# Performance work log

Measured on AMD Instinct MI355X. Metric: run time of the kernel, lower is better.

The kernel has to match this reference:

```python
import jax, jax.numpy as jnp
import numpy as np

N = 100000          # nodes
E = 1200000         # edges
IN_DIM = 128
HID = 64
NUM_CLASSES = 5
NUM_GRAPHS = 128


def setup_inputs() -> dict:
    key = jax.random.key(0)
    ks = jax.random.split(key, 12)
    x = jax.random.normal(ks[0], (N, IN_DIM), dtype=jnp.float32)
    edge_index = jax.random.randint(ks[1], (2, E), 0, N, dtype=jnp.int64)
    batch = jnp.sort(jax.random.randint(ks[2], (N,), 0, NUM_GRAPHS, dtype=jnp.int64))
    def glorot(k, shape):
        lim = np.sqrt(6.0 / (shape[0] + shape[1]))
        return jax.random.uniform(k, shape, jnp.float32, -lim, lim)
    W1 = glorot(ks[3], (IN_DIM, HID)); b1 = jnp.zeros((HID,), jnp.float32)
    W2 = glorot(ks[4], (HID, HID));    b2 = jnp.zeros((HID,), jnp.float32)
    W3 = glorot(ks[5], (HID, HID));    b3 = jnp.zeros((HID,), jnp.float32)
    Wc = glorot(ks[6], (HID, NUM_CLASSES)); bc = jnp.zeros((NUM_CLASSES,), jnp.float32)
    return {"x": x, "edge_index": edge_index, "batch": batch,
            "W1": W1, "b1": b1, "W2": W2, "b2": b2, "W3": W3, "b3": b3,
            "Wc": Wc, "bc": bc}


def _gcn_norm(edge_index, n_nodes):
    # PyG GCNConv: add self-loops, symmetric normalization D^-1/2 (A+I) D^-1/2
    loop = jnp.arange(n_nodes, dtype=edge_index.dtype)
    src = jnp.concatenate([edge_index[0], loop])  # [E+N]
    dst = jnp.concatenate([edge_index[1], loop])
    deg = jax.ops.segment_sum(jnp.ones_like(dst, dtype=jnp.float32), dst,
                              num_segments=n_nodes)
    dinv = jnp.where(deg > 0, jax.lax.rsqrt(deg), 0.0)
    norm = dinv[src] * dinv[dst]                   # [E+N]
    return src, dst, norm


def _gcn_conv(x, src, dst, norm, W, b, n_nodes):
    h = x @ W                                      # [N, out]
    msg = h[src] * norm[:, None]                   # gather + scale
    agg = jax.ops.segment_sum(msg, dst, num_segments=n_nodes)  # scatter-add
    return agg + b


def reference(x, edge_index, batch, W1, b1, W2, b2, W3, b3, Wc, bc):
    src, dst, norm = _gcn_norm(edge_index, N)
    h = jax.nn.relu(_gcn_conv(x, src, dst, norm, W1, b1, N))
    h = jax.nn.relu(_gcn_conv(h, src, dst, norm, W2, b2, N))
    h = jax.nn.relu(_gcn_conv(h, src, dst, norm, W3, b3, N))
    # global_mean_pool over batch ids
    sums = jax.ops.segment_sum(h, batch, num_segments=NUM_GRAPHS)
    counts = jax.ops.segment_sum(jnp.ones((N,), jnp.float32), batch,
                                 num_segments=NUM_GRAPHS)
    pooled = sums / jnp.maximum(counts, 1.0)[:, None]  # [G, HID]
    return pooled @ Wc + bc                             # [G, num_classes]
```

## Files before the change

kernel.cpp:

```cpp
#include <hip/hip_runtime.h>
#include <hip/hip_bf16.h>

#define NN 100000
#define NE 1200000
#define IND 128
#define HID 64
#define NC 5
#define NG 128
#define NB 391
#define GB 1172
#define G1 3125

static __device__ __forceinline__ float bf2f(unsigned short u) {
    union { unsigned int i; float f; } x;
    x.i = (unsigned int)u << 16;
    return x.f;
}
static __device__ __forceinline__ unsigned short f2bf(float f) {
    union { float f; unsigned int i; } x;
    x.f = f;
    unsigned int r = (x.i + 0x7fffu + ((x.i >> 16) & 1u)) >> 16;
    return (unsigned short)r;
}

__global__ __launch_bounds__(256) void k_hist(const int* __restrict__ dst, int* __restrict__ cnt,
                                              int* __restrict__ rank) {
    int e = blockIdx.x * 256 + threadIdx.x;
    if (e < NE) rank[e] = atomicAdd(&cnt[dst[e]], 1);
}

__global__ __launch_bounds__(256) void k_scan1(const int* __restrict__ cnt, int* __restrict__ exc,
                                               int* __restrict__ bsum, float* __restrict__ dinv) {
    __shared__ int lds[256];
    int tid = threadIdx.x;
    int i = blockIdx.x * 256 + tid;
    int v = (i < NN) ? cnt[i] : 0;
    lds[tid] = v;
    __syncthreads();
    for (int off = 1; off < 256; off <<= 1) {
        int t = (tid >= off) ? lds[tid - off] : 0;
        __syncthreads();
        lds[tid] += t;
        __syncthreads();
    }
    if (i < NN) {
        exc[i] = lds[tid] - v;
        dinv[i] = rsqrtf((float)v + 1.0f);
    }
    if (tid == 255) bsum[blockIdx.x] = lds[255];
}

__global__ __launch_bounds__(512) void k_scan2(int* __restrict__ bsum) {
    __shared__ int lds[512];
    int tid = threadIdx.x;
    int v = (tid < NB) ? bsum[tid] : 0;
    lds[tid] = v;
    __syncthreads();
    for (int off = 1; off < 512; off <<= 1) {
        int t = (tid >= off) ? lds[tid - off] : 0;
        __syncthreads();
        lds[tid] += t;
        __syncthreads();
    }
    if (tid < NB) bsum[tid] = lds[tid] - v;
}

__global__ __launch_bounds__(256) void k_scan3(const int* __restrict__ exc, const int* __restrict__ bsum,
                                               int* __restrict__ row_ptr) {
    int i = blockIdx.x * 256 + threadIdx.x;
    if (i < NN) row_ptr[i] = exc[i] + bsum[blockIdx.x];
    if (i == 0) row_ptr[NN] = NE;
}

__global__ __launch_bounds__(256) void k_fused1(
    const float* __restrict__ X, const float* __restrict__ W,
    const float* __restrict__ dinv, unsigned short* __restrict__ out_bf,
    const int* __restrict__ src, const int* __restrict__ dst,
    const int* __restrict__ row_ptr, const int* __restrict__ rank,
    int* __restrict__ src_sorted,
    const int* __restrict__ batch, int* __restrict__ start)
{
    __shared__ float lds[IND * HID + 32 * IND];
    int tid = threadIdx.x;

    if (blockIdx.x < GB) {
        int t = blockIdx.x * 256 + tid;
        const int T = GB * 256;
#pragma unroll
        for (int u = 0; u < 4; ++u) {
            int e = t + u * T;
            if (e < NE) src_sorted[row_ptr[dst[e]] + rank[e]] = src[e];
        }
        return;
    }
    if (blockIdx.x >= GB + G1) {
        int i = (blockIdx.x - GB - G1) * 256 + tid;
        if (i >= NN) return;
        int b = batch[i];
        if (i == 0) {
            for (int g = 0; g <= b; ++g) start[g] = 0;
        } else {
            int p = batch[i - 1];
            for (int g = p + 1; g <= b; ++g) start[g] = i;
        }
        if (i == NN - 1) {
            for (int g = b + 1; g <= NG; ++g) start[g] = NN;
        }
        return;
    }

    float* Wl = lds;
    float* xl = lds + IND * HID;
    int n0 = (blockIdx.x - GB) * 32;
    int c = tid & 31;
    int s = tid >> 5;

    {
        const float4* Wg = (const float4*)W;
        float4* Wl4 = (float4*)Wl;
#pragma unroll
        for (int i = 0; i < IND * 16 / 256; ++i) Wl4[i * 256 + tid] = Wg[i * 256 + tid];
    }
    {
        const float4* Xg = (const float4*)X;
        float4* xl4 = (float4*)xl;
        const float4 z = {0.f, 0.f, 0.f, 0.f};
#pragma unroll
        for (int i = 0; i < 32 * IND / 4 / 256; ++i) {
            int idx = i * 256 + tid;
            int node = n0 + idx / (IND / 4);
            xl4[idx] = (node < NN) ? Xg[(size_t)n0 * (IND / 4) + idx] : z;
        }
    }
    __syncthreads();

    float acc[4][2];
#pragma unroll
    for (int r = 0; r < 4; ++r) { acc[r][0] = 0.f; acc[r][1] = 0.f; }

#pragma unroll 4
    for (int k0 = 0; k0 < IND; k0 += 4) {
        float4 xv[4];
#pragma unroll
        for (int r = 0; r < 4; ++r) xv[r] = *(const float4*)&xl[(s * 4 + r) * IND + k0];
#pragma unroll
        for (int kk = 0; kk < 4; ++kk) {
            float w0 = Wl[(k0 + kk) * HID + c];
            float w1 = Wl[(k0 + kk) * HID + c + 32];
#pragma unroll
            for (int r = 0; r < 4; ++r) {
                float xe = (kk == 0) ? xv[r].x : (kk == 1) ? xv[r].y : (kk == 2) ? xv[r].z : xv[r].w;
                acc[r][0] = fmaf(xe, w0, acc[r][0]);
                acc[r][1] = fmaf(xe, w1, acc[r][1]);
            }
        }
    }

#pragma unroll
    for (int r = 0; r < 4; ++r) {
        int n = n0 + s * 4 + r;
        if (n < NN) {
            float dn = dinv[n];
            out_bf[n * HID + c]      = f2bf(acc[r][0] * dn);
            out_bf[n * HID + c + 32] = f2bf(acc[r][1] * dn);
        }
    }
}

__global__ __launch_bounds__(256) void k_aggregate(const unsigned short* __restrict__ hW,
                                                   const int* __restrict__ srcs,
                                                   const int* __restrict__ row_ptr,
                                                   const float* __restrict__ dinv,
                                                   const float* __restrict__ b,
                                                   unsigned short* __restrict__ outb) {
    int tid = threadIdx.x;
    int j = tid & 63;
    int n = blockIdx.x * 4 + (tid >> 6);
    if (n >= NN) return;
    float acc = bf2f(hW[n * HID + j]);
    int beg = row_ptr[n], end = row_ptr[n + 1];
    int e = beg;
    for (; e + 7 < end; e += 8) {
        int s0 = srcs[e],     s1 = srcs[e + 1], s2 = srcs[e + 2], s3 = srcs[e + 3];
        int s4 = srcs[e + 4], s5 = srcs[e + 5], s6 = srcs[e + 6], s7 = srcs[e + 7];
        float h0 = bf2f(hW[s0 * HID + j]);
        float h1 = bf2f(hW[s1 * HID + j]);
        float h2 = bf2f(hW[s2 * HID + j]);
        float h3 = bf2f(hW[s3 * HID + j]);
        float h4 = bf2f(hW[s4 * HID + j]);
        float h5 = bf2f(hW[s5 * HID + j]);
        float h6 = bf2f(hW[s6 * HID + j]);
        float h7 = bf2f(hW[s7 * HID + j]);
        acc += ((h0 + h1) + (h2 + h3)) + ((h4 + h5) + (h6 + h7));
    }
    if (e + 3 < end) {
        int s0 = srcs[e], s1 = srcs[e + 1], s2 = srcs[e + 2], s3 = srcs[e + 3];
        float h0 = bf2f(hW[s0 * HID + j]);
        float h1 = bf2f(hW[s1 * HID + j]);
        float h2 = bf2f(hW[s2 * HID + j]);
        float h3 = bf2f(hW[s3 * HID + j]);
        acc += (h0 + h1) + (h2 + h3);
        e += 4;
    }
    for (; e < end; ++e) acc += bf2f(hW[srcs[e] * HID + j]);
    outb[n * HID + j] = f2bf(fmaxf(fmaf(dinv[n], acc, b[j]), 0.0f));
}

__global__ __launch_bounds__(256) void k_gemm_bf(const unsigned short* __restrict__ X,
                                                 const float* __restrict__ W,
                                                 const float* __restrict__ dinv,
                                                 unsigned short* __restrict__ outb) {
    __shared__ float Wl[HID * HID];
    __shared__ float xl[64 * HID];
    int tid = threadIdx.x;
    int n0 = blockIdx.x * 64;

    {
        const float4* Wg = (const float4*)W;
        float4* Wl4 = (float4*)Wl;
#pragma unroll
        for (int i = 0; i < HID * HID / 4 / 256; ++i) Wl4[i * 256 + tid] = Wg[i * 256 + tid];
    }
    {
        const uint4* Xg = (const uint4*)X;
#pragma unroll
        for (int i = 0; i < 2; ++i) {
            int idx = i * 256 + tid;
            int ln = idx >> 3;
            int k0 = (idx & 7) * 8;
            int node = n0 + ln;
            float f[8];
            if (node < NN) {
                uint4 u = Xg[(size_t)n0 * 8 + idx];
                f[0] = bf2f((unsigned short)(u.x & 0xffff));
                f[1] = bf2f((unsigned short)(u.x >> 16));
                f[2] = bf2f((unsigned short)(u.y & 0xffff));
                f[3] = bf2f((unsigned short)(u.y >> 16));
                f[4] = bf2f((unsigned short)(u.z & 0xffff));
                f[5] = bf2f((unsigned short)(u.z >> 16));
                f[6] = bf2f((unsigned short)(u.w & 0xffff));
                f[7] = bf2f((unsigned short)(u.w >> 16));
            } else {
#pragma unroll
                for (int q = 0; q < 8; ++q) f[q] = 0.f;
            }
#pragma unroll
            for (int q = 0; q < 8; ++q) xl[ln * HID + k0 + q] = f[q];
        }
    }
    __syncthreads();

    int c = tid & 31;
    int s = tid >> 5;
    float acc[8][2];
#pragma unroll
    for (int r = 0; r < 8; ++r) { acc[r][0] = 0.f; acc[r][1] = 0.f; }

#pragma unroll 4
    for (int k0 = 0; k0 < HID; k0 += 4) {
        float4 xv[8];
#pragma unroll
        for (int r = 0; r < 8; ++r) xv[r] = *(const float4*)&xl[(s * 8 + r) * HID + k0];
#pragma unroll
        for (int kk = 0; kk < 4; ++kk) {
            float w0 = Wl[(k0 + kk) * HID + c];
            float w1 = Wl[(k0 + kk) * HID + c + 32];
#pragma unroll
            for (int r = 0; r < 8; ++r) {
                float xe = (kk == 0) ? xv[r].x : (kk == 1) ? xv[r].y : (kk == 2) ? xv[r].z : xv[r].w;
                acc[r][0] = fmaf(xe, w0, acc[r][0]);
                acc[r][1] = fmaf(xe, w1, acc[r][1]);
            }
        }
    }

#pragma unroll
    for (int r = 0; r < 8; ++r) {
        int n = n0 + s * 8 + r;
        if (n < NN) {
            float dn = dinv[n];
            outb[n * HID + c]      = f2bf(acc[r][0] * dn);
            outb[n * HID + c + 32] = f2bf(acc[r][1] * dn);
        }
    }
}

__global__ __launch_bounds__(256) void k_pool_head(const unsigned short* __restrict__ h,
                                                   const int* __restrict__ start,
                                                   const float* __restrict__ Wc, const float* __restrict__ bc,
                                                   float* __restrict__ out) {
    __shared__ float part[4][HID];
    int g = blockIdx.x;
    int tid = threadIdx.x;
    int j = tid & 63, w = tid >> 6;
    int beg = start[g], end = start[g + 1];
    float acc = 0.0f;
    for (int n = beg + w; n < end; n += 4) acc += bf2f(h[n * HID + j]);
    part[w][j] = acc;
    __syncthreads();
    if (w == 0) {
        float s = part[0][j] + part[1][j] + part[2][j] + part[3][j];
        float cnt = (float)(end - beg);
        float p = s / fmaxf(cnt, 1.0f);
#pragma unroll
        for (int c = 0; c < NC; ++c) {
            float v = p * Wc[j * NC + c];
            for (int off = 32; off > 0; off >>= 1) v += __shfl_down(v, off);
            if (j == 0) out[g * NC + c] = v + bc[c];
        }
    }
}

extern "C" void kernel_launch(void* const* d_in, const int* in_sizes, int n_in,
                              void* d_out, int out_size, void* d_ws, size_t ws_size,
                              hipStream_t stream) {
    const float* x  = (const float*)d_in[0];
    const int* ei   = (const int*)d_in[1];
    const int* bat  = (const int*)d_in[2];
    const float* W1 = (const float*)d_in[3];
    const float* b1 = (const float*)d_in[4];
    const float* W2 = (const float*)d_in[5];
    const float* b2 = (const float*)d_in[6];
    const float* W3 = (const float*)d_in[7];
    const float* b3 = (const float*)d_in[8];
    const float* Wc = (const float*)d_in[9];
    const float* bc = (const float*)d_in[10];
    float* out = (float*)d_out;

    const int* src = ei;
    const int* dst = ei + NE;

    char* wsb = (char*)d_ws;
    float* dinv         = (float*)wsb;
    int*   row_ptr      = (int*)(wsb + 400000);
    int*   srcs         = (int*)(wsb + 800016);
    unsigned short* hWA = (unsigned short*)(wsb + 5600016);
    unsigned short* hWB = (unsigned short*)(wsb + 18400016);
    int*   cnt          = (int*)(wsb + 31200016);
    int*   exc          = (int*)(wsb + 31600016);
    int*   bsum         = (int*)(wsb + 32000016);
    int*   rank         = (int*)(wsb + 32002064);
    int*   start        = (int*)(wsb + 36802064);

    const int gE = (NE + 255) / 256;

    hipMemsetAsync(cnt, 0, NN * sizeof(int), stream);
    k_hist<<<gE, 256, 0, stream>>>(dst, cnt, rank);
    k_scan1<<<NB, 256, 0, stream>>>(cnt, exc, bsum, dinv);
    k_scan2<<<1, 512, 0, stream>>>(bsum);
    k_scan3<<<NB, 256, 0, stream>>>(exc, bsum, row_ptr);

    k_fused1<<<GB + G1 + NB, 256, 0, stream>>>(x, W1, dinv, hWA, src, dst, row_ptr, rank, srcs, bat, start);

    k_aggregate<<<NN / 4, 256, 0, stream>>>(hWA, srcs, row_ptr, dinv, b1, hWB);
    k_gemm_bf<<<(NN + 63) / 64, 256, 0, stream>>>(hWB, W2, dinv, hWA);
    k_aggregate<<<NN / 4, 256, 0, stream>>>(hWA, srcs, row_ptr, dinv, b2, hWB);
    k_gemm_bf<<<(NN + 63) / 64, 256, 0, stream>>>(hWB, W3, dinv, hWA);
    k_aggregate<<<NN / 4, 256, 0, stream>>>(hWA, srcs, row_ptr, dinv, b3, hWB);

    k_pool_head<<<NG, 256, 0, stream>>>(hWB, start, Wc, bc, out);
}
```

Measured before the change: 369.5 us.

## Merge scan passes and split aggregate gathers into packed bf16 pairs across half-wavefronts

Two changes. The second and third scan kernels become one: each block reduces the preceding block sums itself, which removes a single-block launch and a dependency. The aggregate kernel now has each half-wavefront load packed 32-bit bf16 pairs for alternating edges and combines the halves with a cross-lane shuffle. This halves the load instructions per edge and keeps two independent gathers in flight per thread. The cost is the shuffle and the idle half-wave during the epilogue.

Result: faster. 356.0 us (-3.6%).

```diff
diff --git a/kernel.cpp b/kernel.cpp
--- a/kernel.cpp
+++ b/kernel.cpp
@@ -50,25 +50,23 @@
     if (tid == 255) bsum[blockIdx.x] = lds[255];
 }
 
-__global__ __launch_bounds__(512) void k_scan2(int* __restrict__ bsum) {
-    __shared__ int lds[512];
-    int tid = threadIdx.x;
-    int v = (tid < NB) ? bsum[tid] : 0;
+__global__ __launch_bounds__(256) void k_scan23(const int* __restrict__ exc, const int* __restrict__ bsum,
+                                                int* __restrict__ row_ptr) {
+    __shared__ int lds[256];
+    int tid = threadIdx.x;
+    int me = blockIdx.x;
+    int v = 0;
+    if (tid < me) v = bsum[tid];
+    if (tid + 256 < me) v += bsum[tid + 256];
     lds[tid] = v;
     __syncthreads();
-    for (int off = 1; off < 512; off <<= 1) {
-        int t = (tid >= off) ? lds[tid - off] : 0;
+    for (int off = 128; off > 0; off >>= 1) {
+        if (tid < off) lds[tid] += lds[tid + off];
         __syncthreads();
-        lds[tid] += t;
-        __syncthreads();
-    }
-    if (tid < NB) bsum[tid] = lds[tid] - v;
-}
-
-__global__ __launch_bounds__(256) void k_scan3(const int* __restrict__ exc, const int* __restrict__ bsum,
-                                               int* __restrict__ row_ptr) {
-    int i = blockIdx.x * 256 + threadIdx.x;
-    if (i < NN) row_ptr[i] = exc[i] + bsum[blockIdx.x];
+    }
+    int base = lds[0];
+    int i = me * 256 + tid;
+    if (i < NN) row_ptr[i] = exc[i] + base;
     if (i == 0) row_ptr[NN] = NE;
 }
 
@@ -173,37 +171,71 @@
                                                    const float* __restrict__ dinv,
                                                    const float* __restrict__ b,
                                                    unsigned short* __restrict__ outb) {
-    int tid = threadIdx.x;
-    int j = tid & 63;
+    const unsigned int* __restrict__ hW4 = (const unsigned int*)hW;
+    int tid = threadIdx.x;
+    int lane = tid & 63;
+    int half = lane >> 5;
+    int l = lane & 31;
     int n = blockIdx.x * 4 + (tid >> 6);
-    if (n >= NN) return;
-    float acc = bf2f(hW[n * HID + j]);
-    int beg = row_ptr[n], end = row_ptr[n + 1];
-    int e = beg;
+
+    unsigned int su = hW4[(size_t)n * 32 + l];
+    float acc0 = half ? 0.f : bf2f((unsigned short)(su & 0xffff));
+    float acc1 = half ? 0.f : bf2f((unsigned short)(su >> 16));
+
+    int e = row_ptr[n];
+    int end = row_ptr[n + 1];
+
     for (; e + 7 < end; e += 8) {
         int s0 = srcs[e],     s1 = srcs[e + 1], s2 = srcs[e + 2], s3 = srcs[e + 3];
         int s4 = srcs[e + 4], s5 = srcs[e + 5], s6 = srcs[e + 6], s7 = srcs[e + 7];
-        float h0 = bf2f(hW[s0 * HID + j]);
-        float h1 = bf2f(hW[s1 * HID + j]);
-        float h2 = bf2f(hW[s2 * HID + j]);
-        float h3 = bf2f(hW[s3 * HID + j]);
-        float h4 = bf2f(hW[s4 * HID + j]);
-        float h5 = bf2f(hW[s5 * HID + j]);
-        float h6 = bf2f(hW[s6 * HID + j]);
-        float h7 = bf2f(hW[s7 * HID + j]);
-        acc += ((h0 + h1) + (h2 + h3)) + ((h4 + h5) + (h6 + h7));
+        int sa = half ? s1 : s0;
+        int sb = half ? s3 : s2;
+        int sc = half ? s5 : s4;
+        int sd = half ? s7 : s6;
+        unsigned int ua = hW4[(size_t)sa * 32 + l];
+        unsigned int ub = hW4[(size_t)sb * 32 + l];
+        unsigned int uc = hW4[(size_t)sc * 32 + l];
+        unsigned int ud = hW4[(size_t)sd * 32 + l];
+        acc0 += (bf2f((unsigned short)(ua & 0xffff)) + bf2f((unsigned short)(ub & 0xffff)))
+              + (bf2f((unsigned short)(uc & 0xffff)) + bf2f((unsigned short)(ud & 0xffff)));
+        acc1 += (bf2f((unsigned short)(ua >> 16)) + bf2f((unsigned short)(ub >> 16)))
+              + (bf2f((unsigned short)(uc >> 16)) + bf2f((unsigned short)(ud >> 16)));
     }
     if (e + 3 < end) {
         int s0 = srcs[e], s1 = srcs[e + 1], s2 = srcs[e + 2], s3 = srcs[e + 3];
-        float h0 = bf2f(hW[s0 * HID + j]);
-        float h1 = bf2f(hW[s1 * HID + j]);
-        float h2 = bf2f(hW[s2 * HID + j]);
-        float h3 = bf2f(hW[s3 * HID + j]);
-        acc += (h0 + h1) + (h2 + h3);
+        int sa = half ? s1 : s0;
+        int sb = half ? s3 : s2;
+        unsigned int ua = hW4[(size_t)sa * 32 + l];
+        unsigned int ub = hW4[(size_t)sb * 32 + l];
+        acc0 += bf2f((unsigned short)(ua & 0xffff)) + bf2f((unsigned short)(ub & 0xffff));
+        acc1 += bf2f((unsigned short)(ua >> 16)) + bf2f((unsigned short)(ub >> 16));
         e += 4;
     }
-    for (; e < end; ++e) acc += bf2f(hW[srcs[e] * HID + j]);
-    outb[n * HID + j] = f2bf(fmaxf(fmaf(dinv[n], acc, b[j]), 0.0f));
+    if (e + 1 < end) {
+        int s0 = srcs[e], s1 = srcs[e + 1];
+        int sa = half ? s1 : s0;
+        unsigned int ua = hW4[(size_t)sa * 32 + l];
+        acc0 += bf2f((unsigned short)(ua & 0xffff));
+        acc1 += bf2f((unsigned short)(ua >> 16));
+        e += 2;
+    }
+    if (e < end && half == 0) {
+        int s0 = srcs[e];
+        unsigned int ua = hW4[(size_t)s0 * 32 + l];
+        acc0 += bf2f((unsigned short)(ua & 0xffff));
+        acc1 += bf2f((unsigned short)(ua >> 16));
+    }
+
+    acc0 += __shfl_xor(acc0, 32, 64);
+    acc1 += __shfl_xor(acc1, 32, 64);
+
+    if (half == 0) {
+        float dn = dinv[n];
+        float v0 = fmaxf(fmaf(dn, acc0, b[2 * l]), 0.0f);
+        float v1 = fmaxf(fmaf(dn, acc1, b[2 * l + 1]), 0.0f);
+        unsigned int p = (unsigned int)f2bf(v0) | ((unsigned int)f2bf(v1) << 16);
+        ((unsigned int*)outb)[(size_t)n * 32 + l] = p;
+    }
 }
 
 __global__ __launch_bounds__(256) void k_gemm_bf(const unsigned short* __restrict__ X,
@@ -347,8 +379,7 @@
     hipMemsetAsync(cnt, 0, NN * sizeof(int), stream);
     k_hist<<<gE, 256, 0, stream>>>(dst, cnt, rank);
     k_scan1<<<NB, 256, 0, stream>>>(cnt, exc, bsum, dinv);
-    k_scan2<<<1, 512, 0, stream>>>(bsum);
-    k_scan3<<<NB, 256, 0, stream>>>(exc, bsum, row_ptr);
+    k_scan23<<<NB, 256, 0, stream>>>(exc, bsum, row_ptr);
 
     k_fused1<<<GB + G1 + NB, 256, 0, stream>>>(x, W1, dinv, hWA, src, dst, row_ptr, rank, srcs, bat, start);
 
```
